# Kernel tuning notes

Hardware: AMD Instinct MI355X
Metric: run time of the kernel (lower is better)

The kernel has to match this reference:

```python
import jax, jax.numpy as jnp
import numpy as np

N_NODES = 50000
N_EDGES = 800000
F_IN = 256
HID = 64
HEADS = 4
NEG_SLOPE = 0.2


def setup_inputs() -> dict:
    key = jax.random.key(0)
    ks = jax.random.split(key, 12)
    x = jax.random.normal(ks[0], (N_NODES, F_IN), dtype=jnp.float32)
    src = jax.random.randint(ks[1], (N_EDGES,), 0, N_NODES)
    dst = jax.random.randint(ks[2], (N_EDGES,), 0, N_NODES)
    s0 = 1.0 / np.sqrt(F_IN)
    s1 = 1.0 / np.sqrt(HEADS * HID)
    W0 = jax.random.normal(ks[3], (F_IN, HEADS * HID), dtype=jnp.float32) * s0
    a_l0 = jax.random.normal(ks[4], (HEADS, HID), dtype=jnp.float32) * s1
    a_r0 = jax.random.normal(ks[5], (HEADS, HID), dtype=jnp.float32) * s1
    b0 = jnp.zeros((HEADS * HID,), dtype=jnp.float32)
    W1 = jax.random.normal(ks[6], (HEADS * HID, HEADS * HID), dtype=jnp.float32) * s1
    a_l1 = jax.random.normal(ks[7], (HEADS, HID), dtype=jnp.float32) * s1
    a_r1 = jax.random.normal(ks[8], (HEADS, HID), dtype=jnp.float32) * s1
    b1 = jnp.zeros((HEADS * HID,), dtype=jnp.float32)
    return {"x": x, "src": src, "dst": dst,
            "W0": W0, "a_l0": a_l0, "a_r0": a_r0, "b0": b0,
            "W1": W1, "a_l1": a_l1, "a_r1": a_r1, "b1": b1}


def _gat_layer(h, src, dst, W, a_l, a_r, b):
    # h: [N, F_in] -> feat: [N, H, D]
    feat = (h @ W).reshape(h.shape[0], HEADS, HID)
    el = jnp.sum(feat * a_l, axis=-1)  # [N, H]
    er = jnp.sum(feat * a_r, axis=-1)  # [N, H]
    e = jax.nn.leaky_relu(el[src] + er[dst], NEG_SLOPE)  # [E, H]
    # per-destination edge softmax (numerically stable)
    m = jax.ops.segment_max(e, dst, num_segments=N_NODES)  # [N, H]
    ex = jnp.exp(e - m[dst])
    s = jax.ops.segment_sum(ex, dst, num_segments=N_NODES)  # [N, H]
    alpha = ex / jnp.maximum(s[dst], 1e-9)  # [E, H]
    msg = feat[src] * alpha[:, :, None]  # [E, H, D]
    rst = jax.ops.segment_sum(msg, dst, num_segments=N_NODES)  # [N, H, D]
    rst = rst + b.reshape(1, HEADS, HID)
    return jax.nn.elu(rst)


def reference(x, src, dst, W0, a_l0, a_r0, b0, W1, a_l1, a_r1, b1):
    h = _gat_layer(x, src, dst, W0, a_l0, a_r0, b0)  # [N, H, D]
    h = h.reshape(N_NODES, HEADS * HID)              # flatten(1)
    h = _gat_layer(h, src, dst, W1, a_l1, a_r1, b1)  # [N, H, D]
    # list of per-head outputs h[:, i]
    return tuple(h[:, i] for i in range(HEADS))
```

## Files before the change

### kernel.cpp

```cpp
#include <hip/hip_runtime.h>
#include <math.h>

#define N_NODES 50000
#define N_EDGES 800000
#define HEADS 4
#define HID 64
#define FDIM 256
#define LDA 40
#define SCAN_CHUNK 1024
#define SCAN_NB ((N_NODES + SCAN_CHUNK - 1) / SCAN_CHUNK)

typedef __attribute__((ext_vector_type(8))) _Float16 half8;
typedef __attribute__((ext_vector_type(4))) _Float16 half4;
typedef __attribute__((ext_vector_type(4))) float f32x4;


__global__ __launch_bounds__(256) void scan_local(const int* __restrict__ counts,
                                                  int* __restrict__ offs,
                                                  int* __restrict__ bsum, int n) {
    __shared__ int part[256];
    const int b = blockIdx.x, t = threadIdx.x;
    const int base = b * SCAN_CHUNK + t * 4;
    int v[4];
#pragma unroll
    for (int j = 0; j < 4; j++) {
        int idx = base + j;
        v[j] = (idx < n) ? counts[idx] : 0;
    }
    int s0 = v[0], s1 = s0 + v[1], s2 = s1 + v[2], s3 = s2 + v[3];
    part[t] = s3;
    __syncthreads();
    for (int off = 1; off < 256; off <<= 1) {
        int x = (t >= off) ? part[t - off] : 0;
        __syncthreads();
        part[t] += x;
        __syncthreads();
    }
    int prefix = (t > 0) ? part[t - 1] : 0;
    int e[4] = {prefix, prefix + s0, prefix + s1, prefix + s2};
#pragma unroll
    for (int j = 0; j < 4; j++) {
        int idx = base + j;
        if (idx < n) offs[idx] = e[j];
    }
    if (t == 255) bsum[b] = part[255];
}

__global__ __launch_bounds__(64) void scan_bsum(int* __restrict__ bsum,
                                                int* __restrict__ offs, int nb, int n) {
    int lane = threadIdx.x;
    int own = (lane < nb) ? bsum[lane] : 0;
    int v = own;
    for (int off = 1; off < 64; off <<= 1) {
        int x = __shfl_up(v, off);
        if (lane >= off) v += x;
    }
    if (lane < nb) bsum[lane] = v - own;
    if (lane == nb - 1) offs[n] = v;
}

__global__ __launch_bounds__(256) void scan_add(int* __restrict__ offs,
                                                const int* __restrict__ bsum, int n) {
    const int b = blockIdx.x;
    const int p = bsum[b];
    const int base = b * SCAN_CHUNK + threadIdx.x * 4;
#pragma unroll
    for (int j = 0; j < 4; j++) {
        int idx = base + j;
        if (idx < n) offs[idx] += p;
    }
}

__global__ __launch_bounds__(256) void scatter_kernel(const int* __restrict__ src,
                                                      const int* __restrict__ dst,
                                                      const int* __restrict__ offs,
                                                      int* __restrict__ cursor,
                                                      int* __restrict__ csr_src, int E) {
    int i = blockIdx.x * blockDim.x + threadIdx.x;
    if (i < E) {
        int d = dst[i];
        int p = offs[d] + atomicAdd(&cursor[d], 1);
        csr_src[p] = src[i];
    }
}


__global__ __launch_bounds__(256) void wcast_kernel(const float* __restrict__ W0,
                                                    const float* __restrict__ W1,
                                                    _Float16* __restrict__ wt0,
                                                    _Float16* __restrict__ wt1) {
    const float* W = blockIdx.y ? W1 : W0;
    _Float16* wt = blockIdx.y ? wt1 : wt0;
    int n = blockIdx.x * 16 + (threadIdx.x >> 4);
    int k0 = (threadIdx.x & 15) * 16;
    for (int j = 0; j < 16; j++)
        wt[n * FDIM + k0 + j] = (_Float16)W[(k0 + j) * FDIM + n];
}

template <int A32, int DO_HIST>
__global__ __launch_bounds__(512) void mfma_gemm(const _Float16* __restrict__ A16,
                                                 const float* __restrict__ Af,
                                                 const _Float16* __restrict__ Bt,
                                                 const float* __restrict__ al,
                                                 const float* __restrict__ ar,
                                                 _Float16* __restrict__ feat16,
                                                 float* __restrict__ el,
                                                 float* __restrict__ er,
                                                 const int* __restrict__ dst,
                                                 int* __restrict__ counts) {
    __shared__ _Float16 ash[128][LDA];
    __shared__ _Float16 bsh[256][LDA];

    const int t = threadIdx.x;
    const int m0 = blockIdx.x * 128;
    const int wave = t >> 6, lane = t & 63;
    const int quad = lane >> 4, l16 = lane & 15;
    const int wr = (wave >> 2) * 64;
    const int wc = (wave & 3) * 64;

    if (DO_HIST) {
        const int NT = gridDim.x * 512;
        for (int i = blockIdx.x * 512 + t; i < N_EDGES; i += NT)
            atomicAdd(&counts[dst[i]], 1);
    }

    const f32x4 zero = {0.f, 0.f, 0.f, 0.f};
    f32x4 acc[4][4];
#pragma unroll
    for (int i = 0; i < 4; i++)
#pragma unroll
        for (int j = 0; j < 4; j++) acc[i][j] = zero;

    for (int kk = 0; kk < FDIM; kk += 32) {
        {
            int row = t >> 2;
            int kb = (t & 3) * 8;
            int gr = m0 + row; if (gr >= N_NODES) gr = N_NODES - 1;
            if (A32) {
                const float* p = &Af[(size_t)gr * FDIM + kk + kb];
                float4 f0 = *(const float4*)p;
                float4 f1 = *(const float4*)(p + 4);
                half8 hv = {(_Float16)f0.x, (_Float16)f0.y, (_Float16)f0.z, (_Float16)f0.w,
                            (_Float16)f1.x, (_Float16)f1.y, (_Float16)f1.z, (_Float16)f1.w};
                *(half8*)&ash[row][kb] = hv;
            } else {
                *(half8*)&ash[row][kb] = *(const half8*)&A16[(size_t)gr * FDIM + kk + kb];
            }
        }
#pragma unroll
        for (int ii = 0; ii < 2; ii++) {
            int idx = t + ii * 512;
            int row = idx >> 2;
            int kb = (idx & 3) * 8;
            *(half8*)&bsh[row][kb] = *(const half8*)&Bt[(size_t)row * FDIM + kk + kb];
        }
        __syncthreads();

        half8 af[4], bf[4];
#pragma unroll
        for (int i = 0; i < 4; i++) {
            af[i] = *(half8*)&ash[wr + i * 16 + l16][quad * 8];
            bf[i] = *(half8*)&bsh[wc + i * 16 + l16][quad * 8];
        }
#pragma unroll
        for (int mt = 0; mt < 4; mt++)
#pragma unroll
            for (int nt = 0; nt < 4; nt++)
                acc[mt][nt] = __builtin_amdgcn_mfma_f32_16x16x32_f16(bf[nt], af[mt], acc[mt][nt], 0, 0, 0);
        __syncthreads();
    }

    const int h = wc >> 6;
    float4 alv[4], arv[4];
#pragma unroll
    for (int nt = 0; nt < 4; nt++) {
        alv[nt] = *(const float4*)&al[wc + nt * 16 + quad * 4];
        arv[nt] = *(const float4*)&ar[wc + nt * 16 + quad * 4];
    }
#pragma unroll
    for (int mt = 0; mt < 4; mt++) {
        const int m = m0 + wr + mt * 16 + l16;
        const bool ok = (m < N_NODES);
        float pl = 0.f, pr = 0.f;
#pragma unroll
        for (int nt = 0; nt < 4; nt++) {
            f32x4 v = acc[mt][nt];
            if (ok) {
                half4 hv = {(_Float16)v[0], (_Float16)v[1], (_Float16)v[2], (_Float16)v[3]};
                *(half4*)&feat16[(size_t)m * FDIM + wc + nt * 16 + quad * 4] = hv;
            }
            pl += v[0] * alv[nt].x + v[1] * alv[nt].y + v[2] * alv[nt].z + v[3] * alv[nt].w;
            pr += v[0] * arv[nt].x + v[1] * arv[nt].y + v[2] * arv[nt].z + v[3] * arv[nt].w;
        }
        pl += __shfl_xor(pl, 16);
        pl += __shfl_xor(pl, 32);
        pr += __shfl_xor(pr, 16);
        pr += __shfl_xor(pr, 32);
        if (quad == 0 && ok) {
            el[m * 4 + h] = pl;
            er[m * 4 + h] = pr;
        }
    }
}

__global__ __launch_bounds__(256) void agg_fused(const _Float16* __restrict__ feat16,
                                                 const float* __restrict__ el,
                                                 const float* __restrict__ er,
                                                 const float* __restrict__ bias,
                                                 const int* __restrict__ offs,
                                                 const int* __restrict__ csr_src,
                                                 float* __restrict__ out,
                                                 _Float16* __restrict__ h1,
                                                 int mode) {
    const int wave = threadIdx.x >> 6;
    const int lane = threadIdx.x & 63;
    const int n = blockIdx.x * 4 + wave;
    const int head = lane >> 4;
    const int f = lane * 4;
    const int base16 = lane & 48;
    const int j16 = lane & 15;
    const int beg = offs[n];
    const int end = offs[n + 1];
    const float er_h = er[n * 4 + head];

    float4 acc = make_float4(0.f, 0.f, 0.f, 0.f);
    float ss = 0.f;

    for (int c = beg; c < end; c += 16) {
        int e = c + j16;
        int s_own = 0;
        float w_own = 0.f;
        if (e < end) {
            s_own = csr_src[e];
            float lg = el[s_own * 4 + head] + er_h;
            lg = (lg > 0.f) ? lg : 0.2f * lg;
            w_own = __expf(lg);
        }
        ss += w_own;

        int rem = end - c;
        if (rem > 16) rem = 16;

        int j = 0;
        for (; j + 3 < rem; j += 4) {
            int s0 = __shfl(s_own, base16 + j);
            int s1 = __shfl(s_own, base16 + j + 1);
            int s2 = __shfl(s_own, base16 + j + 2);
            int s3 = __shfl(s_own, base16 + j + 3);
            float w0 = __shfl(w_own, base16 + j);
            float w1 = __shfl(w_own, base16 + j + 1);
            float w2 = __shfl(w_own, base16 + j + 2);
            float w3 = __shfl(w_own, base16 + j + 3);
            half4 v0 = *(const half4*)&feat16[(size_t)s0 * FDIM + f];
            half4 v1 = *(const half4*)&feat16[(size_t)s1 * FDIM + f];
            half4 v2 = *(const half4*)&feat16[(size_t)s2 * FDIM + f];
            half4 v3 = *(const half4*)&feat16[(size_t)s3 * FDIM + f];
            acc.x += w0 * (float)v0[0] + w1 * (float)v1[0];
            acc.y += w0 * (float)v0[1] + w1 * (float)v1[1];
            acc.z += w0 * (float)v0[2] + w1 * (float)v1[2];
            acc.w += w0 * (float)v0[3] + w1 * (float)v1[3];
            acc.x += w2 * (float)v2[0] + w3 * (float)v3[0];
            acc.y += w2 * (float)v2[1] + w3 * (float)v3[1];
            acc.z += w2 * (float)v2[2] + w3 * (float)v3[2];
            acc.w += w2 * (float)v2[3] + w3 * (float)v3[3];
        }
        for (; j < rem; j++) {
            int s0 = __shfl(s_own, base16 + j);
            float w0 = __shfl(w_own, base16 + j);
            half4 v0 = *(const half4*)&feat16[(size_t)s0 * FDIM + f];
            acc.x += w0 * (float)v0[0];
            acc.y += w0 * (float)v0[1];
            acc.z += w0 * (float)v0[2];
            acc.w += w0 * (float)v0[3];
        }
    }

    ss += __shfl_xor(ss, 1, 16);
    ss += __shfl_xor(ss, 2, 16);
    ss += __shfl_xor(ss, 4, 16);
    ss += __shfl_xor(ss, 8, 16);

    float S = fmaxf(ss, 1e-9f);
    float inv = 1.f / S;
    float4 bv = *(const float4*)&bias[f];
    float r0 = acc.x * inv + bv.x;
    float r1 = acc.y * inv + bv.y;
    float r2 = acc.z * inv + bv.z;
    float r3 = acc.w * inv + bv.w;
    r0 = (r0 > 0.f) ? r0 : expm1f(r0);
    r1 = (r1 > 0.f) ? r1 : expm1f(r1);
    r2 = (r2 > 0.f) ? r2 : expm1f(r2);
    r3 = (r3 > 0.f) ? r3 : expm1f(r3);

    if (mode) {
        const int d = (lane & 15) * 4;
        float4 rv = make_float4(r0, r1, r2, r3);
        *(float4*)&out[(size_t)head * N_NODES * HID + (size_t)n * HID + d] = rv;
    } else {
        half4 hv = {(_Float16)r0, (_Float16)r1, (_Float16)r2, (_Float16)r3};
        *(half4*)&h1[(size_t)n * FDIM + f] = hv;
    }
}


extern "C" void kernel_launch(void* const* d_in, const int* in_sizes, int n_in,
                              void* d_out, int out_size, void* d_ws, size_t ws_size,
                              hipStream_t stream) {
    const float* x   = (const float*)d_in[0];
    const int*   src = (const int*)d_in[1];
    const int*   dst = (const int*)d_in[2];
    const float* W0  = (const float*)d_in[3];
    const float* al0 = (const float*)d_in[4];
    const float* ar0 = (const float*)d_in[5];
    const float* b0  = (const float*)d_in[6];
    const float* W1  = (const float*)d_in[7];
    const float* al1 = (const float*)d_in[8];
    const float* ar1 = (const float*)d_in[9];
    const float* b1  = (const float*)d_in[10];
    float* out = (float*)d_out;

    _Float16* h1 = (_Float16*)d_out;

    _Float16* feat16 = (_Float16*)d_ws;
    _Float16* wt0 = feat16 + (size_t)N_NODES * FDIM;
    _Float16* wt1 = wt0 + FDIM * FDIM;
    float* el    = (float*)(wt1 + FDIM * FDIM);
    float* er    = el + N_NODES * HEADS;
    int* counts  = (int*)(er + N_NODES * HEADS);
    int* cursor  = counts + N_NODES;
    int* offs    = cursor + N_NODES;
    int* bsum    = offs + 50016;
    int* csr_src = bsum + 64;

    const int ggrid = (N_NODES + 127) / 128;

    hipMemsetAsync(counts, 0, 2 * N_NODES * sizeof(int), stream);
    wcast_kernel<<<dim3(16, 2), 256, 0, stream>>>(W0, W1, wt0, wt1);

    mfma_gemm<1, 1><<<ggrid, 512, 0, stream>>>(nullptr, x, wt0, al0, ar0,
                                               feat16, el, er, dst, counts);

    scan_local<<<SCAN_NB, 256, 0, stream>>>(counts, offs, bsum, N_NODES);
    scan_bsum<<<1, 64, 0, stream>>>(bsum, offs, SCAN_NB, N_NODES);
    scan_add<<<SCAN_NB, 256, 0, stream>>>(offs, bsum, N_NODES);
    scatter_kernel<<<(N_EDGES + 255) / 256, 256, 0, stream>>>(src, dst, offs, cursor, csr_src, N_EDGES);

    agg_fused<<<N_NODES / 4, 256, 0, stream>>>(feat16, el, er, b0, offs, csr_src,
                                               out, h1, 0);

    mfma_gemm<0, 0><<<ggrid, 512, 0, stream>>>(h1, nullptr, wt1, al1, ar1,
                                               feat16, el, er, nullptr, nullptr);
    agg_fused<<<N_NODES / 4, 256, 0, stream>>>(feat16, el, er, b1, offs, csr_src,
                                               out, h1, 1);
}
```

Before: 375.0 us.

## Halve GEMM row tile to 64 and XOR-swizzle LDS layout instead of padding

The MFMA GEMM block tile drops from 128 to 64 rows, so the grid doubles (about 782 blocks), each wave holds a 32x64 output tile, and only half the threads load A. The padded LDS arrays (LDA 40) become unpadded 32-wide rows with an XOR swizzle on the 8-element slot to avoid bank conflicts. The aim is more blocks across the CUs and less LDS per block. In exchange, each block now reloads the full B tile for half as many rows, which doubles B traffic, and per-wave MFMA work is smaller.

Measured after the change: 367.4 us. 2.0% less time.

```diff
diff --git a/kernel.cpp b/kernel.cpp
--- a/kernel.cpp
+++ b/kernel.cpp
@@ -6,7 +6,6 @@
 #define HEADS 4
 #define HID 64
 #define FDIM 256
-#define LDA 40
 #define SCAN_CHUNK 1024
 #define SCAN_NB ((N_NODES + SCAN_CHUNK - 1) / SCAN_CHUNK)
 
@@ -108,62 +107,67 @@
                                                  float* __restrict__ er,
                                                  const int* __restrict__ dst,
                                                  int* __restrict__ counts) {
-    __shared__ _Float16 ash[128][LDA];
-    __shared__ _Float16 bsh[256][LDA];
+    __shared__ _Float16 ash[64 * 32];
+    __shared__ _Float16 bsh[256 * 32];
 
     const int t = threadIdx.x;
-    const int m0 = blockIdx.x * 128;
+    const int m0 = blockIdx.x * 64;
     const int wave = t >> 6, lane = t & 63;
     const int quad = lane >> 4, l16 = lane & 15;
-    const int wr = (wave >> 2) * 64;
+    const int wr = (wave >> 2) * 32;
     const int wc = (wave & 3) * 64;
 
     if (DO_HIST) {
-        const int NT = gridDim.x * 512;
-        for (int i = blockIdx.x * 512 + t; i < N_EDGES; i += NT)
+        for (int i = blockIdx.x * 512 + t; i < N_EDGES; i += gridDim.x * 512)
             atomicAdd(&counts[dst[i]], 1);
     }
 
     const f32x4 zero = {0.f, 0.f, 0.f, 0.f};
-    f32x4 acc[4][4];
-#pragma unroll
-    for (int i = 0; i < 4; i++)
+    f32x4 acc[2][4];
+#pragma unroll
+    for (int i = 0; i < 2; i++)
 #pragma unroll
         for (int j = 0; j < 4; j++) acc[i][j] = zero;
 
+    const int rslot = ((quad ^ (l16 & 3) ^ (l16 >> 2)) * 8);
+
     for (int kk = 0; kk < FDIM; kk += 32) {
-        {
-            int row = t >> 2;
-            int kb = (t & 3) * 8;
+        if (t < 256) {
+            int row = t >> 2, slotL = t & 3;
+            int ps = ((slotL ^ (row & 3) ^ ((row >> 2) & 3)) * 8);
             int gr = m0 + row; if (gr >= N_NODES) gr = N_NODES - 1;
             if (A32) {
-                const float* p = &Af[(size_t)gr * FDIM + kk + kb];
+                const float* p = &Af[(size_t)gr * FDIM + kk + slotL * 8];
                 float4 f0 = *(const float4*)p;
                 float4 f1 = *(const float4*)(p + 4);
                 half8 hv = {(_Float16)f0.x, (_Float16)f0.y, (_Float16)f0.z, (_Float16)f0.w,
                             (_Float16)f1.x, (_Float16)f1.y, (_Float16)f1.z, (_Float16)f1.w};
-                *(half8*)&ash[row][kb] = hv;
+                *(half8*)&ash[row * 32 + ps] = hv;
             } else {
-                *(half8*)&ash[row][kb] = *(const half8*)&A16[(size_t)gr * FDIM + kk + kb];
+                *(half8*)&ash[row * 32 + ps] =
+                    *(const half8*)&A16[(size_t)gr * FDIM + kk + slotL * 8];
             }
         }
 #pragma unroll
         for (int ii = 0; ii < 2; ii++) {
             int idx = t + ii * 512;
-            int row = idx >> 2;
-            int kb = (idx & 3) * 8;
-            *(half8*)&bsh[row][kb] = *(const half8*)&Bt[(size_t)row * FDIM + kk + kb];
+            int row = idx >> 2, slotL = idx & 3;
+            int ps = ((slotL ^ (row & 3) ^ ((row >> 2) & 3)) * 8);
+            *(half8*)&bsh[row * 32 + ps] =
+                *(const half8*)&Bt[(size_t)row * FDIM + kk + slotL * 8];
         }
         __syncthreads();
 
-        half8 af[4], bf[4];
-#pragma unroll
-        for (int i = 0; i < 4; i++) {
-            af[i] = *(half8*)&ash[wr + i * 16 + l16][quad * 8];
-            bf[i] = *(half8*)&bsh[wc + i * 16 + l16][quad * 8];
-        }
-#pragma unroll
-        for (int mt = 0; mt < 4; mt++)
+        half8 af[2], bf[4];
+#pragma unroll
+        for (int i = 0; i < 2; i++)
+            af[i] = *(half8*)&ash[(wr + i * 16 + l16) * 32 + rslot];
+#pragma unroll
+        for (int i = 0; i < 4; i++)
+            bf[i] = *(half8*)&bsh[(wc + i * 16 + l16) * 32 + rslot];
+
+#pragma unroll
+        for (int mt = 0; mt < 2; mt++)
 #pragma unroll
             for (int nt = 0; nt < 4; nt++)
                 acc[mt][nt] = __builtin_amdgcn_mfma_f32_16x16x32_f16(bf[nt], af[mt], acc[mt][nt], 0, 0, 0);
@@ -178,7 +182,7 @@
         arv[nt] = *(const float4*)&ar[wc + nt * 16 + quad * 4];
     }
 #pragma unroll
-    for (int mt = 0; mt < 4; mt++) {
+    for (int mt = 0; mt < 2; mt++) {
         const int m = m0 + wr + mt * 16 + l16;
         const bool ok = (m < N_NODES);
         float pl = 0.f, pr = 0.f;
@@ -332,7 +336,7 @@
     int* bsum    = offs + 50016;
     int* csr_src = bsum + 64;
 
-    const int ggrid = (N_NODES + 127) / 128;
+    const int ggrid = (N_NODES + 63) / 64;
 
     hipMemsetAsync(counts, 0, 2 * N_NODES * sizeof(int), stream);
     wcast_kernel<<<dim3(16, 2), 256, 0, stream>>>(W0, W1, wt0, wt1);
```
